# Optimization experiments

Hardware: AMD Instinct MI355X
Metric: run time of the kernel (lower is better)

The kernel has to match this reference:

```python
import jax, jax.numpy as jnp
import numpy as np

DIM = 512
HEADS = 8
DIM_HEAD = 64
DIM_INNER = HEADS * DIM_HEAD
FRAC_GRAD = 0.5
SCALE = DIM_HEAD ** -0.5
EPS_CUMPROD = 1e-10
EPS_INV = 1e-8


def setup_inputs() -> dict:
    key = jax.random.key(0)
    ks = jax.random.split(key, 8)
    b, n = 2, 2048
    x = jax.random.normal(ks[0], (b, n, DIM), dtype=jnp.float32)
    gamma = jnp.ones((DIM,), dtype=jnp.float32)
    w_qkv = jax.random.normal(ks[1], (DIM, 3 * DIM_INNER), dtype=jnp.float32) * 0.02
    b_qkv = jnp.zeros((3 * DIM_INNER,), dtype=jnp.float32)
    # to_a: torch init is zeros weight + bias 10; use small random weight and
    # moderate bias so the decay gate is non-trivial for correctness testing
    w_a = jax.random.normal(ks[2], (DIM, DIM_INNER), dtype=jnp.float32) * 0.02
    b_a = jnp.full((DIM_INNER,), 2.0, dtype=jnp.float32)
    w_out = jax.random.normal(ks[3], (DIM_INNER, DIM), dtype=jnp.float32) * 0.02
    b_out = jnp.zeros((DIM,), dtype=jnp.float32)
    return {"x": x, "gamma": gamma, "w_qkv": w_qkv, "b_qkv": b_qkv,
            "w_a": w_a, "b_a": b_a, "w_out": w_out, "b_out": b_out}


def _rms_norm(x, gamma):
    # F.normalize(x, dim=-1) * sqrt(dim) * gamma
    nrm = jnp.linalg.norm(x, axis=-1, keepdims=True)
    return x / jnp.maximum(nrm, 1e-12) * (DIM ** 0.5) * gamma


def _safe_cumprod(t, axis):
    t = jnp.clip(t, EPS_CUMPROD, 1.0)
    return jnp.exp(jnp.cumsum(jnp.log(t), axis=axis))


def reference(x, gamma, w_qkv, b_qkv, w_a, b_a, w_out, b_out):
    b, n, _ = x.shape
    x = _rms_norm(x, gamma)

    qkv = x @ w_qkv + b_qkv  # [b, n, 3*h*d]
    qkv = qkv.reshape(b, n, 3, HEADS, DIM_HEAD).transpose(2, 0, 3, 1, 4)  # [3,b,h,n,d]
    q, k, v = qkv[0], qkv[1], qkv[2]
    q = q * SCALE

    # data-dependent relative-position decay gate
    a = (x @ w_a + b_a).reshape(b, n, HEADS, DIM_HEAD).transpose(0, 2, 1, 3)  # [b,h,n,d]
    a = a * FRAC_GRAD + jax.lax.stop_gradient(a) * (1.0 - FRAC_GRAD)
    a = jax.nn.sigmoid(a)
    a_cum = _safe_cumprod(a, axis=-2)
    a_cum_inv = 1.0 / jnp.maximum(a_cum, EPS_INV)

    q = q * a_cum
    k = k * a_cum_inv

    sim = jnp.einsum('bhid,bhjd->bhij', q, k)
    causal_mask = jnp.triu(jnp.ones((n, n), dtype=bool), k=1)
    attn = jnp.where(causal_mask, 0.0, sim)  # no softmax in decay branch

    out = jnp.einsum('bhij,bhjd->bhid', attn, v)  # [b,h,n,d]
    out = out.transpose(0, 2, 1, 3).reshape(b, n, DIM_INNER)
    return out @ w_out + b_out
```

## Files before the change

kernel.cpp:

```cpp
#include <hip/hip_runtime.h>


using s8v   = __attribute__((ext_vector_type(8))) short;
using f32x4 = __attribute__((ext_vector_type(4))) float;

__device__ __forceinline__ unsigned short f2b(float f) {
  unsigned int u = __builtin_bit_cast(unsigned int, f);
  u += 0x7FFFu + ((u >> 16) & 1u);
  return (unsigned short)(u >> 16);
}
__device__ __forceinline__ float b2f(unsigned short b) {
  unsigned int u = ((unsigned int)b) << 16;
  return __builtin_bit_cast(float, u);
}

__device__ __forceinline__ f32x4 mfma16(s8v a, s8v b, f32x4 c) {
  return __builtin_amdgcn_mfma_f32_16x16x32_bf16(a, b, c, 0, 0, 0);
}

__device__ __forceinline__ void gload16(const void* g, void* l) {
  __builtin_amdgcn_global_load_lds(
      (const __attribute__((address_space(1))) void*)g,
      (__attribute__((address_space(3))) void*)l, 16, 0, 0);
}

__global__ __launch_bounds__(256) void prep_k(const float* __restrict__ x,
                                              const float* __restrict__ gamma,
                                              short* __restrict__ xnb,
                                              const float* __restrict__ w_qkv,
                                              const float* __restrict__ w_a,
                                              const float* __restrict__ w_out,
                                              short* __restrict__ wT,
                                              short* __restrict__ woT) {
  __shared__ float t[32][33];
  int bid = blockIdx.x;
  if (bid < 1024) {
    int row  = bid * 4 + (threadIdx.x >> 6);
    int lane = threadIdx.x & 63;
    const float4* xp = reinterpret_cast<const float4*>(x + (size_t)row * 512 + lane * 8);
    float4 v0 = xp[0], v1 = xp[1];
    float ss = v0.x*v0.x + v0.y*v0.y + v0.z*v0.z + v0.w*v0.w
             + v1.x*v1.x + v1.y*v1.y + v1.z*v1.z + v1.w*v1.w;
#pragma unroll
    for (int off = 32; off > 0; off >>= 1) ss += __shfl_xor(ss, off, 64);
    float s = 22.627416997969522f / fmaxf(sqrtf(ss), 1e-12f);
    const float* g = gamma + lane * 8;
    float vals[8] = {v0.x, v0.y, v0.z, v0.w, v1.x, v1.y, v1.z, v1.w};
    s8v o;
#pragma unroll
    for (int j = 0; j < 8; ++j) o[j] = (short)f2b(vals[j] * s * g[j]);
    *reinterpret_cast<s8v*>(xnb + (size_t)row * 512 + lane * 8) = o;
  } else {
    int id = bid - 1024;
    int bx = id % 80, k0 = (id / 80) * 32;
    const float* src; short* dst; int N, n0;
    if (bx < 48)      { src = w_qkv; dst = wT;                      N = 1536; n0 = bx * 32; }
    else if (bx < 64) { src = w_a;   dst = wT + (size_t)1536 * 512; N = 512;  n0 = (bx - 48) * 32; }
    else              { src = w_out; dst = woT;                     N = 512;  n0 = (bx - 64) * 32; }
    int tx = threadIdx.x & 31, ty = threadIdx.x >> 5;
#pragma unroll
    for (int i = 0; i < 4; ++i)
      t[ty + 8 * i][tx] = src[(size_t)(k0 + ty + 8 * i) * N + n0 + tx];
    __syncthreads();
#pragma unroll
    for (int i = 0; i < 4; ++i)
      dst[(size_t)(n0 + ty + 8 * i) * 512 + k0 + tx] = (short)f2b(t[tx][ty + 8 * i]);
  }
}

template <int BM, int BN, int EPI>
__global__ __launch_bounds__(256) void gemm_bt(const short* __restrict__ A,
                                               const short* __restrict__ Bm,
                                               void* __restrict__ Cout,
                                               const float* __restrict__ bias0,
                                               const float* __restrict__ bias1,
                                               float* __restrict__ araw,
                                               float* __restrict__ csum,
                                               int M, int N, int K) {
  __shared__ __align__(16) char LA[BM * 128];
  __shared__ __align__(16) char LB[BN * 128];
  constexpr int WM = BM / 2, WN = BN / 2, FM = WM / 16, FN = WN / 16;
  const int tid = threadIdx.x, lane = tid & 63, wave = tid >> 6;
  const int wr = (wave >> 1) * WM, wc = (wave & 1) * WN;
  int orig = blockIdx.y * gridDim.x + blockIdx.x;
  int xcd = orig & 7, rq = orig >> 3;
  int bx = rq % gridDim.x;
  int by = xcd * (gridDim.y >> 3) + rq / gridDim.x;
  const int m0 = by * BM, n0 = bx * BN;
  const int NS = K / 64;

  auto stage = [&](int k0) {
#pragma unroll
    for (int r = 0; r < BM / 32; ++r) {
      int o = r * 4096 + tid * 16;
      int row = o >> 7;
      int ce = (((o & 127) ^ ((row & 7) << 4)) >> 1);
      gload16(A + (size_t)(m0 + row) * K + k0 + ce, LA + o);
    }
#pragma unroll
    for (int r = 0; r < BN / 32; ++r) {
      int o = r * 4096 + tid * 16;
      int row = o >> 7;
      int ce = (((o & 127) ^ ((row & 7) << 4)) >> 1);
      gload16(Bm + (size_t)(n0 + row) * K + k0 + ce, LB + o);
    }
  };

  f32x4 acc[FM][FN] = {};
  for (int t = 0; t < NS; ++t) {
    stage(t * 64);
    __syncthreads();
#pragma unroll
    for (int kk = 0; kk < 2; ++kk) {
      s8v af[FM], bf[FN];
#pragma unroll
      for (int m = 0; m < FM; ++m) {
        int row = wr + m * 16 + (lane & 15);
        int ad = ((row << 7) + kk * 64 + ((lane >> 4) << 4)) ^ ((row & 7) << 4);
        af[m] = *reinterpret_cast<const s8v*>(LA + ad);
      }
#pragma unroll
      for (int n = 0; n < FN; ++n) {
        int row = wc + n * 16 + (lane & 15);
        int ad = ((row << 7) + kk * 64 + ((lane >> 4) << 4)) ^ ((row & 7) << 4);
        bf[n] = *reinterpret_cast<const s8v*>(LB + ad);
      }
#pragma unroll
      for (int m = 0; m < FM; ++m)
#pragma unroll
        for (int n = 0; n < FN; ++n)
          acc[m][n] = mfma16(af[m], bf[n], acc[m][n]);
    }
    if (t + 1 < NS) __syncthreads();
  }

  if constexpr (EPI == 0) {
    short* qkvb = (short*)Cout;
    if (n0 < 1536) {
#pragma unroll
      for (int m = 0; m < FM; ++m)
#pragma unroll
        for (int n = 0; n < FN; ++n)
#pragma unroll
          for (int r = 0; r < 4; ++r) {
            int row = m0 + wr + m * 16 + ((lane >> 4) << 2) + r;
            int col = n0 + wc + n * 16 + (lane & 15);
            float v = acc[m][n][r] + bias0[col];
            int w = col >> 9, h = (col >> 6) & 7, d = col & 63;
            int b = row >> 11, nn = row & 2047;
            qkvb[((((size_t)(w * 2 + b)) * 8 + h) * 2048 + nn) * 64 + d] = (short)f2b(v);
          }
    } else {
      float cs[FN] = {};
      int b = m0 >> 11;
#pragma unroll
      for (int m = 0; m < FM; ++m)
#pragma unroll
        for (int n = 0; n < FN; ++n)
#pragma unroll
          for (int r = 0; r < 4; ++r) {
            int row = m0 + wr + m * 16 + ((lane >> 4) << 2) + r;
            int gc = n0 + wc + n * 16 + (lane & 15) - 1536;
            int h = gc >> 6, d = gc & 63, nn = row & 2047;
            float xv = acc[m][n][r] + bias1[gc];
            araw[((size_t)(b * 8 + h) * 2048 + nn) * 64 + d] = xv;
            float a = 1.f / (1.f + expf(-xv));
            a = fminf(fmaxf(a, 1e-10f), 1.f);
            cs[n] += logf(a);
          }
#pragma unroll
      for (int n = 0; n < FN; ++n) {
        cs[n] += __shfl_xor(cs[n], 16, 64);
        cs[n] += __shfl_xor(cs[n], 32, 64);
      }
      int nsel = lane >> 4;
      float v = (nsel == 0) ? cs[0] : (nsel == 1) ? cs[1] : (nsel == 2) ? cs[2] : cs[3];
      int col = wc + nsel * 16 + (lane & 15);
      int gc = n0 + col - 1536;
      int h = gc >> 6, d = gc & 63;
      int chunkg = ((m0 & 2047) >> 6) + (wave >> 1);
      csum[(((size_t)(b * 8 + h)) * 32 + chunkg) * 64 + d] = v;
    }
  } else {
    float* C = (float*)Cout;
#pragma unroll
    for (int m = 0; m < FM; ++m)
#pragma unroll
      for (int n = 0; n < FN; ++n)
#pragma unroll
        for (int r = 0; r < 4; ++r) {
          int row = m0 + wr + m * 16 + ((lane >> 4) << 2) + r;
          int col = n0 + wc + n * 16 + (lane & 15);
          C[(size_t)row * N + col] = acc[m][n][r] + bias0[col];
        }
  }
}

__global__ __launch_bounds__(256) void scan2_k(const short* __restrict__ qkvb,
                                               const float* __restrict__ araw,
                                               const float* __restrict__ csum,
                                               short* __restrict__ q2,
                                               short* __restrict__ k2,
                                               short* __restrict__ vT,
                                               short* __restrict__ Sbuf) {
  int chunk = blockIdx.x, bh = blockIdx.y;
  int tid = threadIdx.x, lane = tid & 63, wave = tid >> 6;
  int d = lane;
  __shared__ short kL[64][72], vL[64][72];
  __shared__ float wsum[4][64];
  __shared__ __align__(16) char kT[8192], vTl[8192];
  float pre = 0.f;
  for (int c = 0; c < chunk; ++c) pre += csum[((size_t)bh * 32 + c) * 64 + d];
  const float* ap = araw + ((size_t)bh * 2048 + chunk * 64 + wave * 16) * 64 + d;
  float la[16]; float run = 0.f;
#pragma unroll
  for (int rr = 0; rr < 16; ++rr) {
    float xv = ap[rr * 64];
    float a = 1.f / (1.f + expf(-xv));
    a = fminf(fmaxf(a, 1e-10f), 1.f);
    run += logf(a);
    la[rr] = run;
  }
  wsum[wave][d] = run;
  __syncthreads();
#pragma unroll
  for (int w = 0; w < 3; ++w) if (w < wave) pre += wsum[w][d];
  const size_t WS = (size_t)2 * 8 * 2048 * 64;
  size_t base = ((size_t)bh * 2048 + chunk * 64 + wave * 16) * 64 + d;
#pragma unroll 4
  for (int rr = 0; rr < 16; ++rr) {
    int r = wave * 16 + rr;
    float g = expf(pre + la[rr]);
    float gi = 1.f / fmaxf(g, 1e-8f);
    float qv = b2f((unsigned short)qkvb[base + rr * 64]);
    float kv = b2f((unsigned short)qkvb[base + WS + rr * 64]);
    short vb = qkvb[base + 2 * WS + rr * 64];
    q2[base + rr * 64] = (short)f2b(qv * 0.125f * g);
    unsigned short kb = f2b(kv * gi);
    k2[base + rr * 64] = (short)kb;
    kL[r][d] = (short)kb;
    vL[r][d] = vb;
  }
  __syncthreads();
  short* vTrow = vT + ((size_t)bh * 64 + d) * 2048 + chunk * 64;
#pragma unroll
  for (int gg = 0; gg < 2; ++gg) {
    int g8 = wave + gg * 4;
    s8v pk, pv;
#pragma unroll
    for (int j = 0; j < 8; ++j) { pk[j] = kL[g8 * 8 + j][d]; pv[j] = vL[g8 * 8 + j][d]; }
    *reinterpret_cast<s8v*>(vTrow + g8 * 8) = pv;
    int ad = ((d << 7) + g8 * 16) ^ ((d & 7) << 4);
    *reinterpret_cast<s8v*>(kT  + ad) = pk;
    *reinterpret_cast<s8v*>(vTl + ad) = pv;
  }
  __syncthreads();
  f32x4 acc[4] = {};
#pragma unroll
  for (int kk = 0; kk < 2; ++kk) {
    int arow = wave * 16 + (lane & 15);
    int aad = ((arow << 7) + kk * 64 + ((lane >> 4) << 4)) ^ ((arow & 7) << 4);
    s8v av = *reinterpret_cast<const s8v*>(vTl + aad);
#pragma unroll
    for (int n = 0; n < 4; ++n) {
      int brow = n * 16 + (lane & 15);
      int bad = ((brow << 7) + kk * 64 + ((lane >> 4) << 4)) ^ ((brow & 7) << 4);
      acc[n] = mfma16(av, *reinterpret_cast<const s8v*>(kT + bad), acc[n]);
    }
  }
  short* Sp = Sbuf + ((size_t)bh * 32 + chunk) * 4096;
#pragma unroll
  for (int n = 0; n < 4; ++n)
#pragma unroll
    for (int r = 0; r < 4; ++r)
      Sp[(wave * 16 + ((lane >> 4) << 2) + r) * 64 + n * 16 + (lane & 15)] = (short)f2b(acc[n][r]);
}

__global__ __launch_bounds__(256) void sprefix_k(const short* __restrict__ Sbuf,
                                                 short* __restrict__ Spre) {
  int bh = blockIdx.x >> 4;
  int e = ((blockIdx.x & 15) << 8) + threadIdx.x;
  size_t base = (size_t)bh * 32 * 4096 + e;
  float acc = 0.f;
  for (int c = 0; c < 32; ++c) {
    Spre[base + (size_t)c * 4096] = (short)f2b(acc);
    acc += b2f((unsigned short)Sbuf[base + (size_t)c * 4096]);
  }
}

__global__ __launch_bounds__(256) void attnk_k(const short* __restrict__ q2,
                                               const short* __restrict__ k2,
                                               const short* __restrict__ vT,
                                               const short* __restrict__ Spre,
                                               short* __restrict__ aout) {
  int chunk = blockIdx.x, bh = blockIdx.y;
  int tid = threadIdx.x, lane = tid & 63, wave = tid >> 6;
  __shared__ __align__(16) char LQ[8192], LK[8192], LV[8192], LS[8192], LP[8192];
#pragma unroll
  for (int rr = 0; rr < 2; ++rr) {
    int o = rr * 4096 + tid * 16;
    int row = o >> 7;
    int ce = (((o & 127) ^ ((row & 7) << 4)) >> 1);
    gload16(q2   + ((size_t)bh * 2048 + chunk * 64 + row) * 64 + ce, LQ + o);
    gload16(k2   + ((size_t)bh * 2048 + chunk * 64 + row) * 64 + ce, LK + o);
    gload16(vT   + ((size_t)bh * 64 + row) * 2048 + chunk * 64 + ce, LV + o);
    gload16(Spre + (((size_t)bh * 32 + chunk) * 64 + row) * 64 + ce, LS + o);
  }
  __syncthreads();
  f32x4 accS[4] = {}, accO[4] = {};
#pragma unroll
  for (int kk = 0; kk < 2; ++kk) {
    int arow = wave * 16 + (lane & 15);
    int aad = ((arow << 7) + kk * 64 + ((lane >> 4) << 4)) ^ ((arow & 7) << 4);
    s8v aq = *reinterpret_cast<const s8v*>(LQ + aad);
#pragma unroll
    for (int n = 0; n < 4; ++n) {
      int brow = n * 16 + (lane & 15);
      int bad = ((brow << 7) + kk * 64 + ((lane >> 4) << 4)) ^ ((brow & 7) << 4);
      accS[n] = mfma16(aq, *reinterpret_cast<const s8v*>(LK + bad), accS[n]);
      accO[n] = mfma16(aq, *reinterpret_cast<const s8v*>(LS + bad), accO[n]);
    }
  }
#pragma unroll
  for (int n = 0; n < 4; ++n)
#pragma unroll
    for (int r = 0; r < 4; ++r) {
      int i = wave * 16 + ((lane >> 4) << 2) + r;
      int j = n * 16 + (lane & 15);
      float v = (j <= i) ? accS[n][r] : 0.f;
      int ad = ((i << 7) + (j << 1)) ^ ((i & 7) << 4);
      *reinterpret_cast<short*>(LP + ad) = (short)f2b(v);
    }
  __syncthreads();
#pragma unroll
  for (int kk = 0; kk < 2; ++kk) {
    int arow = wave * 16 + (lane & 15);
    int aad = ((arow << 7) + kk * 64 + ((lane >> 4) << 4)) ^ ((arow & 7) << 4);
    s8v ap = *reinterpret_cast<const s8v*>(LP + aad);
#pragma unroll
    for (int n = 0; n < 4; ++n) {
      int brow = n * 16 + (lane & 15);
      int bad = ((brow << 7) + kk * 64 + ((lane >> 4) << 4)) ^ ((brow & 7) << 4);
      accO[n] = mfma16(ap, *reinterpret_cast<const s8v*>(LV + bad), accO[n]);
    }
  }
  int b = bh >> 3, h = bh & 7;
#pragma unroll
  for (int n = 0; n < 4; ++n)
#pragma unroll
    for (int r = 0; r < 4; ++r) {
      int i = wave * 16 + ((lane >> 4) << 2) + r;
      int col = h * 64 + n * 16 + (lane & 15);
      size_t row = (size_t)b * 2048 + chunk * 64 + i;
      aout[row * 512 + col] = (short)f2b(accO[n][r]);
    }
}

extern "C" void kernel_launch(void* const* d_in, const int* in_sizes, int n_in,
                              void* d_out, int out_size, void* d_ws, size_t ws_size,
                              hipStream_t stream) {
  const float* x     = (const float*)d_in[0];
  const float* gamma = (const float*)d_in[1];
  const float* w_qkv = (const float*)d_in[2];
  const float* b_qkv = (const float*)d_in[3];
  const float* w_a   = (const float*)d_in[4];
  const float* b_a   = (const float*)d_in[5];
  const float* w_out = (const float*)d_in[6];
  const float* b_out = (const float*)d_in[7];
  float* out = (float*)d_out;
  char* ws = (char*)d_ws;

  const size_t MB = 1u << 20;
  short* xnb  = (short*)(ws);
  short* wT   = (short*)(ws + 4  * MB);
  short* woT  = (short*)(ws + 6  * MB);
  short* qkvb = (short*)(ws + 7  * MB);
  float* araw = (float*)(ws + 19 * MB);
  float* csum = (float*)(ws + 27 * MB);
  short* q2   = (short*)(ws + 28 * MB);
  short* k2   = (short*)(ws + 32 * MB);
  short* vT   = (short*)(ws + 36 * MB);
  short* Sbuf = (short*)(ws + 40 * MB);
  short* Spre = (short*)(ws + 44 * MB);
  short* aout = (short*)(ws + 48 * MB);

  prep_k<<<2304, 256, 0, stream>>>(x, gamma, xnb, w_qkv, w_a, w_out, wT, woT);

  gemm_bt<128, 128, 0><<<dim3(16, 32), 256, 0, stream>>>(
      xnb, wT, qkvb, b_qkv, b_a, araw, csum, 4096, 2048, 512);

  scan2_k<<<dim3(32, 16), 256, 0, stream>>>(qkvb, araw, csum, q2, k2, vT, Sbuf);

  sprefix_k<<<256, 256, 0, stream>>>(Sbuf, Spre);
  attnk_k<<<dim3(32, 16), 256, 0, stream>>>(q2, k2, vT, Spre, aout);

  gemm_bt<64, 64, 1><<<dim3(8, 64), 256, 0, stream>>>(
      aout, woT, out, b_out, b_out, nullptr, nullptr, 4096, 512, 512);
}
```

Baseline: 71.14 us.

## Fuse all stages into one cooperative persistent kernel with grid syncs

Merges the six separate kernels (prep, QKV GEMM, scan, prefix, chunk attention, output GEMM) into one cooperative kernel of 512 blocks that separates stages with grid-wide syncs. Each stage uses a shared 32KB LDS arena, and the attention stage reuses the Q buffer for P to save LDS. The aim is to remove the launch gaps between kernels. The cost is grid.sync overhead, a residency limit of two blocks per CU, and register pressure from the largest stage. A fallback path launches the separate kernels if the cooperative launch fails.

```diff
diff --git a/kernel.cpp b/kernel.cpp
--- a/kernel.cpp
+++ b/kernel.cpp
@@ -1,5 +1,8 @@
 #include <hip/hip_runtime.h>
-
+#include <hip/hip_cooperative_groups.h>
+
+
+namespace cg = cooperative_groups;
 
 using s8v   = __attribute__((ext_vector_type(8))) short;
 using f32x4 = __attribute__((ext_vector_type(4))) float;
@@ -13,30 +16,24 @@
   unsigned int u = ((unsigned int)b) << 16;
   return __builtin_bit_cast(float, u);
 }
-
 __device__ __forceinline__ f32x4 mfma16(s8v a, s8v b, f32x4 c) {
   return __builtin_amdgcn_mfma_f32_16x16x32_bf16(a, b, c, 0, 0, 0);
 }
-
 __device__ __forceinline__ void gload16(const void* g, void* l) {
   __builtin_amdgcn_global_load_lds(
       (const __attribute__((address_space(1))) void*)g,
       (__attribute__((address_space(3))) void*)l, 16, 0, 0);
 }
 
-__global__ __launch_bounds__(256) void prep_k(const float* __restrict__ x,
-                                              const float* __restrict__ gamma,
-                                              short* __restrict__ xnb,
-                                              const float* __restrict__ w_qkv,
-                                              const float* __restrict__ w_a,
-                                              const float* __restrict__ w_out,
-                                              short* __restrict__ wT,
-                                              short* __restrict__ woT) {
-  __shared__ float t[32][33];
-  int bid = blockIdx.x;
-  if (bid < 1024) {
-    int row  = bid * 4 + (threadIdx.x >> 6);
-    int lane = threadIdx.x & 63;
+__device__ __forceinline__ void st_prep(int u, int tid, char* arena,
+    const float* __restrict__ x, const float* __restrict__ gamma,
+    short* __restrict__ xnb,
+    const float* __restrict__ w_qkv, const float* __restrict__ w_a,
+    const float* __restrict__ w_out,
+    short* __restrict__ wT, short* __restrict__ woT) {
+  int lane = tid & 63, wave = tid >> 6;
+  if (u < 1024) {
+    int row = u * 4 + wave;
     const float4* xp = reinterpret_cast<const float4*>(x + (size_t)row * 512 + lane * 8);
     float4 v0 = xp[0], v1 = xp[1];
     float ss = v0.x*v0.x + v0.y*v0.y + v0.z*v0.z + v0.w*v0.w
@@ -51,13 +48,15 @@
     for (int j = 0; j < 8; ++j) o[j] = (short)f2b(vals[j] * s * g[j]);
     *reinterpret_cast<s8v*>(xnb + (size_t)row * 512 + lane * 8) = o;
   } else {
-    int id = bid - 1024;
+    float (*t)[33] = reinterpret_cast<float (*)[33]>(arena);
+    int id = u - 1024;
     int bx = id % 80, k0 = (id / 80) * 32;
     const float* src; short* dst; int N, n0;
     if (bx < 48)      { src = w_qkv; dst = wT;                      N = 1536; n0 = bx * 32; }
     else if (bx < 64) { src = w_a;   dst = wT + (size_t)1536 * 512; N = 512;  n0 = (bx - 48) * 32; }
     else              { src = w_out; dst = woT;                     N = 512;  n0 = (bx - 64) * 32; }
-    int tx = threadIdx.x & 31, ty = threadIdx.x >> 5;
+    int tx = tid & 31, ty = tid >> 5;
+    __syncthreads();
 #pragma unroll
     for (int i = 0; i < 4; ++i)
       t[ty + 8 * i][tx] = src[(size_t)(k0 + ty + 8 * i) * N + n0 + tx];
@@ -68,47 +67,31 @@
   }
 }
 
-template <int BM, int BN, int EPI>
-__global__ __launch_bounds__(256) void gemm_bt(const short* __restrict__ A,
-                                               const short* __restrict__ Bm,
-                                               void* __restrict__ Cout,
-                                               const float* __restrict__ bias0,
-                                               const float* __restrict__ bias1,
-                                               float* __restrict__ araw,
-                                               float* __restrict__ csum,
-                                               int M, int N, int K) {
-  __shared__ __align__(16) char LA[BM * 128];
-  __shared__ __align__(16) char LB[BN * 128];
-  constexpr int WM = BM / 2, WN = BN / 2, FM = WM / 16, FN = WN / 16;
-  const int tid = threadIdx.x, lane = tid & 63, wave = tid >> 6;
-  const int wr = (wave >> 1) * WM, wc = (wave & 1) * WN;
-  int orig = blockIdx.y * gridDim.x + blockIdx.x;
-  int xcd = orig & 7, rq = orig >> 3;
-  int bx = rq % gridDim.x;
-  int by = xcd * (gridDim.y >> 3) + rq / gridDim.x;
-  const int m0 = by * BM, n0 = bx * BN;
-  const int NS = K / 64;
-
-  auto stage = [&](int k0) {
+template <int BM, int BN, int FM, int FN>
+__device__ __forceinline__ void gemm_core(const short* __restrict__ A,
+                                          const short* __restrict__ Bm,
+                                          char* LA, char* LB,
+                                          int m0, int n0, int tid,
+                                          f32x4 (&acc)[FM][FN]) {
+  const int lane = tid & 63, wave = tid >> 6;
+  const int wr = (wave >> 1) * (BM / 2), wc = (wave & 1) * (BN / 2);
+#pragma unroll 1
+  for (int t = 0; t < 8; ++t) {
+    const int k0 = t * 64;
 #pragma unroll
     for (int r = 0; r < BM / 32; ++r) {
       int o = r * 4096 + tid * 16;
       int row = o >> 7;
       int ce = (((o & 127) ^ ((row & 7) << 4)) >> 1);
-      gload16(A + (size_t)(m0 + row) * K + k0 + ce, LA + o);
+      gload16(A + (size_t)(m0 + row) * 512 + k0 + ce, LA + o);
     }
 #pragma unroll
     for (int r = 0; r < BN / 32; ++r) {
       int o = r * 4096 + tid * 16;
       int row = o >> 7;
       int ce = (((o & 127) ^ ((row & 7) << 4)) >> 1);
-      gload16(Bm + (size_t)(n0 + row) * K + k0 + ce, LB + o);
-    }
-  };
-
-  f32x4 acc[FM][FN] = {};
-  for (int t = 0; t < NS; ++t) {
-    stage(t * 64);
+      gload16(Bm + (size_t)(n0 + row) * 512 + k0 + ce, LB + o);
+    }
     __syncthreads();
 #pragma unroll
     for (int kk = 0; kk < 2; ++kk) {
@@ -131,84 +114,80 @@
         for (int n = 0; n < FN; ++n)
           acc[m][n] = mfma16(af[m], bf[n], acc[m][n]);
     }
-    if (t + 1 < NS) __syncthreads();
-  }
-
-  if constexpr (EPI == 0) {
-    short* qkvb = (short*)Cout;
-    if (n0 < 1536) {
-#pragma unroll
-      for (int m = 0; m < FM; ++m)
-#pragma unroll
-        for (int n = 0; n < FN; ++n)
-#pragma unroll
-          for (int r = 0; r < 4; ++r) {
-            int row = m0 + wr + m * 16 + ((lane >> 4) << 2) + r;
-            int col = n0 + wc + n * 16 + (lane & 15);
-            float v = acc[m][n][r] + bias0[col];
-            int w = col >> 9, h = (col >> 6) & 7, d = col & 63;
-            int b = row >> 11, nn = row & 2047;
-            qkvb[((((size_t)(w * 2 + b)) * 8 + h) * 2048 + nn) * 64 + d] = (short)f2b(v);
-          }
-    } else {
-      float cs[FN] = {};
-      int b = m0 >> 11;
-#pragma unroll
-      for (int m = 0; m < FM; ++m)
-#pragma unroll
-        for (int n = 0; n < FN; ++n)
-#pragma unroll
-          for (int r = 0; r < 4; ++r) {
-            int row = m0 + wr + m * 16 + ((lane >> 4) << 2) + r;
-            int gc = n0 + wc + n * 16 + (lane & 15) - 1536;
-            int h = gc >> 6, d = gc & 63, nn = row & 2047;
-            float xv = acc[m][n][r] + bias1[gc];
-            araw[((size_t)(b * 8 + h) * 2048 + nn) * 64 + d] = xv;
-            float a = 1.f / (1.f + expf(-xv));
-            a = fminf(fmaxf(a, 1e-10f), 1.f);
-            cs[n] += logf(a);
-          }
-#pragma unroll
-      for (int n = 0; n < FN; ++n) {
-        cs[n] += __shfl_xor(cs[n], 16, 64);
-        cs[n] += __shfl_xor(cs[n], 32, 64);
-      }
-      int nsel = lane >> 4;
-      float v = (nsel == 0) ? cs[0] : (nsel == 1) ? cs[1] : (nsel == 2) ? cs[2] : cs[3];
-      int col = wc + nsel * 16 + (lane & 15);
-      int gc = n0 + col - 1536;
-      int h = gc >> 6, d = gc & 63;
-      int chunkg = ((m0 & 2047) >> 6) + (wave >> 1);
-      csum[(((size_t)(b * 8 + h)) * 32 + chunkg) * 64 + d] = v;
-    }
-  } else {
-    float* C = (float*)Cout;
-#pragma unroll
-    for (int m = 0; m < FM; ++m)
-#pragma unroll
-      for (int n = 0; n < FN; ++n)
+    if (t + 1 < 8) __syncthreads();
+  }
+}
+
+__device__ __forceinline__ void st_gemm0(int vid, int tid, char* arena,
+    const short* __restrict__ xnb, const short* __restrict__ wT,
+    short* __restrict__ qkvb, const float* __restrict__ b_qkv,
+    const float* __restrict__ b_a, float* __restrict__ araw,
+    float* __restrict__ csum) {
+  const int lane = tid & 63, wave = tid >> 6;
+  int xcd = vid & 7, rq = vid >> 3;
+  int bx = rq & 15, by = xcd * 4 + (rq >> 4);
+  int m0 = by * 128, n0 = bx * 128;
+  f32x4 acc[4][4] = {};
+  gemm_core<128, 128, 4, 4>(xnb, wT, arena, arena + 16384, m0, n0, tid, acc);
+  int wr = (wave >> 1) * 64, wc = (wave & 1) * 64;
+  if (n0 < 1536) {
+#pragma unroll
+    for (int m = 0; m < 4; ++m)
+#pragma unroll
+      for (int n = 0; n < 4; ++n)
 #pragma unroll
         for (int r = 0; r < 4; ++r) {
           int row = m0 + wr + m * 16 + ((lane >> 4) << 2) + r;
           int col = n0 + wc + n * 16 + (lane & 15);
-          C[(size_t)row * N + col] = acc[m][n][r] + bias0[col];
+          float v = acc[m][n][r] + b_qkv[col];
+          int w = col >> 9, h = (col >> 6) & 7, d = col & 63;
+          int b = row >> 11, nn = row & 2047;
+          qkvb[((((size_t)(w * 2 + b)) * 8 + h) * 2048 + nn) * 64 + d] = (short)f2b(v);
         }
-  }
-}
-
-__global__ __launch_bounds__(256) void scan2_k(const short* __restrict__ qkvb,
-                                               const float* __restrict__ araw,
-                                               const float* __restrict__ csum,
-                                               short* __restrict__ q2,
-                                               short* __restrict__ k2,
-                                               short* __restrict__ vT,
-                                               short* __restrict__ Sbuf) {
-  int chunk = blockIdx.x, bh = blockIdx.y;
-  int tid = threadIdx.x, lane = tid & 63, wave = tid >> 6;
-  int d = lane;
-  __shared__ short kL[64][72], vL[64][72];
-  __shared__ float wsum[4][64];
-  __shared__ __align__(16) char kT[8192], vTl[8192];
+  } else {
+    float cs[4] = {};
+    int b = m0 >> 11;
+#pragma unroll
+    for (int m = 0; m < 4; ++m)
+#pragma unroll
+      for (int n = 0; n < 4; ++n)
+#pragma unroll
+        for (int r = 0; r < 4; ++r) {
+          int row = m0 + wr + m * 16 + ((lane >> 4) << 2) + r;
+          int gc = n0 + wc + n * 16 + (lane & 15) - 1536;
+          int h = gc >> 6, d = gc & 63, nn = row & 2047;
+          float xv = acc[m][n][r] + b_a[gc];
+          araw[((size_t)(b * 8 + h) * 2048 + nn) * 64 + d] = xv;
+          float a = 1.f / (1.f + expf(-xv));
+          a = fminf(fmaxf(a, 1e-10f), 1.f);
+          cs[n] += logf(a);
+        }
+#pragma unroll
+    for (int n = 0; n < 4; ++n) {
+      cs[n] += __shfl_xor(cs[n], 16, 64);
+      cs[n] += __shfl_xor(cs[n], 32, 64);
+    }
+    int nsel = lane >> 4;
+    float v = (nsel == 0) ? cs[0] : (nsel == 1) ? cs[1] : (nsel == 2) ? cs[2] : cs[3];
+    int col = wc + nsel * 16 + (lane & 15);
+    int gc = n0 + col - 1536;
+    int h = gc >> 6, d = gc & 63;
+    int chunkg = ((m0 & 2047) >> 6) + (wave >> 1);
+    csum[(((size_t)(b * 8 + h)) * 32 + chunkg) * 64 + d] = v;
+  }
+}
+
+__device__ __forceinline__ void st_scan2(int vid, int tid, char* arena,
+    const short* __restrict__ qkvb, const float* __restrict__ araw,
+    const float* __restrict__ csum, short* __restrict__ q2,
+    short* __restrict__ k2, short* __restrict__ vT, short* __restrict__ Sbuf) {
+  int chunk = vid & 31, bh = vid >> 5;
+  int lane = tid & 63, wave = tid >> 6, d = lane;
+  short (*kL)[64] = reinterpret_cast<short (*)[64]>(arena);
+  short (*vL)[64] = reinterpret_cast<short (*)[64]>(arena + 8192);
+  char* kT  = arena + 16384;
+  char* vTl = arena + 24576;
+  float (*wsum)[64] = reinterpret_cast<float (*)[64]>(arena + 16384);
   float pre = 0.f;
   for (int c = 0; c < chunk; ++c) pre += csum[((size_t)bh * 32 + c) * 64 + d];
   const float* ap = araw + ((size_t)bh * 2048 + chunk * 64 + wave * 16) * 64 + d;
@@ -276,10 +255,10 @@
       Sp[(wave * 16 + ((lane >> 4) << 2) + r) * 64 + n * 16 + (lane & 15)] = (short)f2b(acc[n][r]);
 }
 
-__global__ __launch_bounds__(256) void sprefix_k(const short* __restrict__ Sbuf,
-                                                 short* __restrict__ Spre) {
-  int bh = blockIdx.x >> 4;
-  int e = ((blockIdx.x & 15) << 8) + threadIdx.x;
+__device__ __forceinline__ void st_sprefix(int vid, int tid,
+    const short* __restrict__ Sbuf, short* __restrict__ Spre) {
+  int bh = vid >> 4;
+  int e = ((vid & 15) << 8) + tid;
   size_t base = (size_t)bh * 32 * 4096 + e;
   float acc = 0.f;
   for (int c = 0; c < 32; ++c) {
@@ -288,14 +267,16 @@
   }
 }
 
-__global__ __launch_bounds__(256) void attnk_k(const short* __restrict__ q2,
-                                               const short* __restrict__ k2,
-                                               const short* __restrict__ vT,
-                                               const short* __restrict__ Spre,
-                                               short* __restrict__ aout) {
-  int chunk = blockIdx.x, bh = blockIdx.y;
-  int tid = threadIdx.x, lane = tid & 63, wave = tid >> 6;
-  __shared__ __align__(16) char LQ[8192], LK[8192], LV[8192], LS[8192], LP[8192];
+__device__ __forceinline__ void st_attnk(int vid, int tid, char* arena,
+    const short* __restrict__ q2, const short* __restrict__ k2,
+    const short* __restrict__ vT, const short* __restrict__ Spre,
+    short* __restrict__ aout) {
+  int chunk = vid & 31, bh = vid >> 5;
+  int lane = tid & 63, wave = tid >> 6;
+  char* LQ = arena;
+  char* LK = arena + 8192;
+  char* LV = arena + 16384;
+  char* LS = arena + 24576;
 #pragma unroll
   for (int rr = 0; rr < 2; ++rr) {
     int o = rr * 4096 + tid * 16;
@@ -321,6 +302,7 @@
       accO[n] = mfma16(aq, *reinterpret_cast<const s8v*>(LS + bad), accO[n]);
     }
   }
+  __syncthreads();
 #pragma unroll
   for (int n = 0; n < 4; ++n)
 #pragma unroll
@@ -329,14 +311,14 @@
       int j = n * 16 + (lane & 15);
       float v = (j <= i) ? accS[n][r] : 0.f;
       int ad = ((i << 7) + (j << 1)) ^ ((i & 7) << 4);
-      *reinterpret_cast<short*>(LP + ad) = (short)f2b(v);
+      *reinterpret_cast<short*>(LQ + ad) = (short)f2b(v);
     }
   __syncthreads();
 #pragma unroll
   for (int kk = 0; kk < 2; ++kk) {
     int arow = wave * 16 + (lane & 15);
     int aad = ((arow << 7) + kk * 64 + ((lane >> 4) << 4)) ^ ((arow & 7) << 4);
-    s8v ap = *reinterpret_cast<const s8v*>(LP + aad);
+    s8v ap = *reinterpret_cast<const s8v*>(LQ + aad);
 #pragma unroll
     for (int n = 0; n < 4; ++n) {
       int brow = n * 16 + (lane & 15);
@@ -354,6 +336,91 @@
       size_t row = (size_t)b * 2048 + chunk * 64 + i;
       aout[row * 512 + col] = (short)f2b(accO[n][r]);
     }
+}
+
+__device__ __forceinline__ void st_gemm1(int vid, int tid, char* arena,
+    const short* __restrict__ aout, const short* __restrict__ woT,
+    float* __restrict__ out, const float* __restrict__ b_out) {
+  const int lane = tid & 63, wave = tid >> 6;
+  int xcd = vid & 7, rq = vid >> 3;
+  int bx = rq & 7, by = xcd * 8 + (rq >> 3);
+  int m0 = by * 64, n0 = bx * 64;
+  f32x4 acc[2][2] = {};
+  gemm_core<64, 64, 2, 2>(aout, woT, arena, arena + 8192, m0, n0, tid, acc);
+  int wr = (wave >> 1) * 32, wc = (wave & 1) * 32;
+#pragma unroll
+  for (int m = 0; m < 2; ++m)
+#pragma unroll
+    for (int n = 0; n < 2; ++n)
+#pragma unroll
+      for (int r = 0; r < 4; ++r) {
+        int row = m0 + wr + m * 16 + ((lane >> 4) << 2) + r;
+        int col = n0 + wc + n * 16 + (lane & 15);
+        out[(size_t)row * 512 + col] = acc[m][n][r] + b_out[col];
+      }
+}
+
+__global__ __launch_bounds__(256, 2) void mega_k(
+    const float* __restrict__ x, const float* __restrict__ gamma,
+    const float* __restrict__ w_qkv, const float* __restrict__ b_qkv,
+    const float* __restrict__ w_a, const float* __restrict__ b_a,
+    const float* __restrict__ w_out, const float* __restrict__ b_out,
+    float* __restrict__ out,
+    short* __restrict__ xnb, short* __restrict__ wT, short* __restrict__ woT,
+    short* __restrict__ qkvb, float* __restrict__ araw, float* __restrict__ csum,
+    short* __restrict__ q2, short* __restrict__ k2, short* __restrict__ vT,
+    short* __restrict__ Sbuf, short* __restrict__ Spre, short* __restrict__ aout) {
+  __shared__ __align__(16) char arena[32768];
+  cg::grid_group grid = cg::this_grid();
+  const int bid = blockIdx.x, tid = threadIdx.x;
+
+  for (int u = bid; u < 2304; u += 512)
+    st_prep(u, tid, arena, x, gamma, xnb, w_qkv, w_a, w_out, wT, woT);
+  __threadfence(); grid.sync();
+
+  st_gemm0(bid, tid, arena, xnb, wT, qkvb, b_qkv, b_a, araw, csum);
+  __threadfence(); grid.sync();
+
+  st_scan2(bid, tid, arena, qkvb, araw, csum, q2, k2, vT, Sbuf);
+  __threadfence(); grid.sync();
+
+  if (bid < 256) st_sprefix(bid, tid, Sbuf, Spre);
+  __threadfence(); grid.sync();
+
+  st_attnk(bid, tid, arena, q2, k2, vT, Spre, aout);
+  __threadfence(); grid.sync();
+
+  st_gemm1(bid, tid, arena, aout, woT, out, b_out);
+}
+
+__global__ __launch_bounds__(256) void prep_k(const float* x, const float* gamma,
+    short* xnb, const float* w_qkv, const float* w_a, const float* w_out,
+    short* wT, short* woT) {
+  __shared__ __align__(16) char arena[4224];
+  st_prep(blockIdx.x, threadIdx.x, arena, x, gamma, xnb, w_qkv, w_a, w_out, wT, woT);
+}
+__global__ __launch_bounds__(256) void gemm0_k(const short* xnb, const short* wT,
+    short* qkvb, const float* b_qkv, const float* b_a, float* araw, float* csum) {
+  __shared__ __align__(16) char arena[32768];
+  st_gemm0(blockIdx.x, threadIdx.x, arena, xnb, wT, qkvb, b_qkv, b_a, araw, csum);
+}
+__global__ __launch_bounds__(256) void scan2_k(const short* qkvb, const float* araw,
+    const float* csum, short* q2, short* k2, short* vT, short* Sbuf) {
+  __shared__ __align__(16) char arena[32768];
+  st_scan2(blockIdx.x, threadIdx.x, arena, qkvb, araw, csum, q2, k2, vT, Sbuf);
+}
+__global__ __launch_bounds__(256) void sprefix_k(const short* Sbuf, short* Spre) {
+  st_sprefix(blockIdx.x, threadIdx.x, Sbuf, Spre);
+}
+__global__ __launch_bounds__(256) void attnk_k(const short* q2, const short* k2,
+    const short* vT, const short* Spre, short* aout) {
+  __shared__ __align__(16) char arena[32768];
+  st_attnk(blockIdx.x, threadIdx.x, arena, q2, k2, vT, Spre, aout);
+}
+__global__ __launch_bounds__(256) void gemm1_k(const short* aout, const short* woT,
+    float* out, const float* b_out) {
+  __shared__ __align__(16) char arena[16384];
+  st_gemm1(blockIdx.x, threadIdx.x, arena, aout, woT, out, b_out);
 }
 
 extern "C" void kernel_launch(void* const* d_in, const int* in_sizes, int n_in,
@@ -384,16 +451,25 @@
   short* Spre = (short*)(ws + 44 * MB);
   short* aout = (short*)(ws + 48 * MB);
 
-  prep_k<<<2304, 256, 0, stream>>>(x, gamma, xnb, w_qkv, w_a, w_out, wT, woT);
-
-  gemm_bt<128, 128, 0><<<dim3(16, 32), 256, 0, stream>>>(
-      xnb, wT, qkvb, b_qkv, b_a, araw, csum, 4096, 2048, 512);
-
-  scan2_k<<<dim3(32, 16), 256, 0, stream>>>(qkvb, araw, csum, q2, k2, vT, Sbuf);
-
-  sprefix_k<<<256, 256, 0, stream>>>(Sbuf, Spre);
-  attnk_k<<<dim3(32, 16), 256, 0, stream>>>(q2, k2, vT, Spre, aout);
-
-  gemm_bt<64, 64, 1><<<dim3(8, 64), 256, 0, stream>>>(
-      aout, woT, out, b_out, b_out, nullptr, nullptr, 4096, 512, 512);
-}
+  int dev = 0; (void)hipGetDevice(&dev);
+  int coop = 0;
+  (void)hipDeviceGetAttribute(&coop, hipDeviceAttributeCooperativeLaunch, dev);
+  int nb = 0;
+  (void)hipOccupancyMaxActiveBlocksPerMultiprocessor(&nb, mega_k, 256, 0);
+
+  hipError_t err = hipErrorUnknown;
+  if (coop && nb >= 2) {
+    void* args[] = {&x, &gamma, &w_qkv, &b_qkv, &w_a, &b_a, &w_out, &b_out,
+                    &out, &xnb, &wT, &woT, &qkvb, &araw, &csum,
+                    &q2, &k2, &vT, &Sbuf, &Spre, &aout};
+    err = hipLaunchCooperativeKernel((void*)mega_k, dim3(512), dim3(256), args, 0, stream);
+  }
+  if (err != hipSuccess) {
+    prep_k   <<<2304, 256, 0, stream>>>(x, gamma, xnb, w_qkv, w_a, w_out, wT, woT);
+    gemm0_k  <<<512,  256, 0, stream>>>(xnb, wT, qkvb, b_qkv, b_a, araw, csum);
+    scan2_k  <<<512,  256, 0, stream>>>(qkvb, araw, csum, q2, k2, vT, Sbuf);
+    sprefix_k<<<256,  256, 0, stream>>>(Sbuf, Spre);
+    attnk_k  <<<512,  256, 0, stream>>>(q2, k2, vT, Spre, aout);
+    gemm1_k  <<<512,  256, 0, stream>>>(aout, woT, out, b_out);
+  }
+}
```

Measured after the change: 70.98 us. About the same (-0.2%).
